# Kernel tuning notes

Hardware: AMD Instinct MI355X
Metric: run time of the kernel (lower is better)

## Reference

```python
import jax, jax.numpy as jnp
import numpy as np

B, IN_DIM, HID, N, ORDER = 128, 2, 64, 1024, 2
NUM_SUPPORTS = 2
IN_TOT = (IN_DIM + HID) * (ORDER * NUM_SUPPORTS + 1)  # 66*5 = 330


def setup_inputs() -> dict:
    key = jax.random.key(0)
    ks = jax.random.split(key, 6)
    inputs = jax.random.normal(ks[0], (B, IN_DIM, N), jnp.float32)
    hx = jax.random.normal(ks[1], (B, HID, N), jnp.float32)
    # row-stochastic-ish diffusion supports, scaled for numerical sanity
    A0 = jax.random.uniform(ks[2], (N, N), jnp.float32) * (2.0 / N)
    A1 = jax.random.uniform(ks[3], (N, N), jnp.float32) * (2.0 / N)
    # 1x1 Conv1d weights (squeezed kernel dim): (out_ch, in_ch)
    W_ru = jax.random.normal(ks[4], (2 * HID, IN_TOT), jnp.float32) * 0.05
    b_ru = jnp.ones((2 * HID,), jnp.float32)  # bias_start=1.0
    W_C = jax.random.normal(ks[5], (HID, IN_TOT), jnp.float32) * 0.05
    b_C = jnp.zeros((HID,), jnp.float32)  # bias_start=0.0
    return {"inputs": inputs, "hx": hx, "A0": A0, "A1": A1,
            "W_ru": W_ru, "b_ru": b_ru, "W_C": W_C, "b_C": b_C}


def _gcn(x, A, order):
    # Chebyshev-like diffusion recursion; x: (B, F, N), A: (N, N)
    x0 = x
    x1 = jnp.einsum('bfn,mn->bfm', x0, A)
    out = [x1]
    for _ in range(2, order + 1):
        x2 = 2.0 * jnp.einsum('bfn,mn->bfm', x1, A) - x0
        out.append(x2)
        x1, x0 = x2, x1
    return jnp.concatenate(out, axis=-2)  # (B, F*order, N)


def _multi_adj_gnn(x, adjs, W, b, order):
    # concat identity + per-support diffusion stacks, then 1x1 conv over channels
    h = jnp.concatenate([x] + [_gcn(x, A, order) for A in adjs], axis=-2)
    return jnp.einsum('bcn,oc->bon', h, W) + b[None, :, None]


def reference(inputs, hx, A0, A1, W_ru, b_ru, W_C, b_C):
    adjs = (A0, A1)
    x = jnp.concatenate([inputs, hx], axis=-2)            # (B, IN+HID, N)
    ru = jax.nn.sigmoid(_multi_adj_gnn(x, adjs, W_ru, b_ru, ORDER))
    r, u = ru[:, :HID, :], ru[:, HID:, :]
    xc = jnp.concatenate([inputs, r * hx], axis=-2)
    Cc = jnp.tanh(_multi_adj_gnn(xc, adjs, W_C, b_C, ORDER))
    return u * hx + (1.0 - u) * Cc                        # (B, HID, N)
```

## Files before the change

kernel.cpp:

```cpp
#include <hip/hip_runtime.h>

using u16 = unsigned short;
using u32 = unsigned int;
typedef __attribute__((ext_vector_type(8))) __bf16 bf16x8;
typedef __attribute__((ext_vector_type(8))) u16 u16x8;
typedef __attribute__((ext_vector_type(4))) float f32x4;

#define DEVI __device__ __forceinline__

constexpr int BN_ = 128;
constexpr int NN  = 1024;
constexpr int CH  = 66;
constexpr int HD  = 64;
constexpr int RR  = BN_ * CH;
constexpr long RN = (long)RR * NN;
constexpr int KTRUE = 330, KPAD = 352;
constexpr long M2 = (long)NN * NN;

DEVI float bf2f(u16 u) { u32 i = ((u32)u) << 16; float f; __builtin_memcpy(&f, &i, 4); return f; }
DEVI u16 f2bf(float f) { u32 i; __builtin_memcpy(&i, &f, 4); i += 0x7fffu + ((i >> 16) & 1u); return (u16)(i >> 16); }

DEVI void gl_lds16(const void* g, void* l) {
  __builtin_amdgcn_global_load_lds((const __attribute__((address_space(1))) u32*)g,
                                   (__attribute__((address_space(3))) u32*)l, 16, 0, 0);
}

template<bool CHEB>
__global__ __launch_bounds__(256, 2)
void gemm_bt(const u16* __restrict__ Xb, long xz,
             const u16* __restrict__ Ab,
             const u16* __restrict__ X0,
             u16* __restrict__ Yb, long yz)
{
  __shared__ u16 Xs[128 * 32];
  __shared__ u16 Bs[128 * 32];
  const int bid = blockIdx.x;
  const int wg  = (bid & 7) * 132 + (bid >> 3);
  const int z   = wg >= 528;
  const int rem = wg - z * 528;
  const int tm  = rem >> 3, tn = rem & 7;

  const u16* X = Xb + (long)z * xz;
  const u16* A = Ab + (long)z * M2;
  u16*       Y = Yb + (long)z * yz;
  const int tid = threadIdx.x, wv = tid >> 6, ln = tid & 63;

  const int r0  = wv * 16 + (ln >> 2);
  const int kch = (((ln & 3) ^ ((r0 >> 1) & 3))) * 8;
  const u16* gX = X + (long)(tm * 128 + r0) * NN + kch;
  const u16* gA = A + (long)(tn * 128 + r0) * NN + kch;
  u16* lX = &Xs[wv * 512];
  u16* lA = &Bs[wv * 512];

  const int frow = ln & 15;
  const int fk   = ((ln >> 4) ^ ((ln >> 1) & 3)) * 8;
  const int wr = wv >> 1, wc = wv & 1;

  f32x4 acc[4][4] = {};

  for (int k0 = 0; k0 < NN; k0 += 32) {
    gl_lds16(gX + k0,            lX);
    gl_lds16(gX + k0 + 64 * NN,  lX + 2048);
    gl_lds16(gA + k0,            lA);
    gl_lds16(gA + k0 + 64 * NN,  lA + 2048);
    __syncthreads();
    bf16x8 af[4], bfv[4];
#pragma unroll
    for (int m = 0; m < 4; m++) af[m]  = *(const bf16x8*)&Xs[(wr * 64 + m * 16 + frow) * 32 + fk];
#pragma unroll
    for (int n = 0; n < 4; n++) bfv[n] = *(const bf16x8*)&Bs[(wc * 64 + n * 16 + frow) * 32 + fk];
#pragma unroll
    for (int m = 0; m < 4; m++)
#pragma unroll
      for (int n = 0; n < 4; n++)
        acc[m][n] = __builtin_amdgcn_mfma_f32_16x16x32_bf16(af[m], bfv[n], acc[m][n], 0, 0, 0);
    __syncthreads();
  }

  const int colb = tn * 128 + wc * 64 + frow;
  const int rowb = tm * 128 + wr * 64 + (ln >> 4) * 4;
#pragma unroll
  for (int m = 0; m < 4; m++)
#pragma unroll
    for (int n = 0; n < 4; n++) {
      const int col = colb + n * 16;
#pragma unroll
      for (int q = 0; q < 4; q++) {
        const long r = rowb + m * 16 + q;
        float v = acc[m][n][q];
        if (CHEB) v = 2.0f * v - bf2f(X0[r * NN + col]);
        Y[r * NN + col] = f2bf(v);
      }
    }
}

template<int O, bool FINAL>
__global__ __launch_bounds__(512)
void proj_f(const u16* __restrict__ part0, const u16* __restrict__ Yb,
            const u16* __restrict__ W, const float* __restrict__ bias,
            const float* __restrict__ hx, const u16* __restrict__ zpad,
            u16* __restrict__ xcrow, float* __restrict__ ubuf,
            float* __restrict__ outp)
{
  __shared__ u16 LB[23040];
  __shared__ u16 LA[5632];
  const int b = blockIdx.y, n0 = blockIdx.x * 64;
  const int tid = threadIdx.x, wv = tid >> 6, ln = tid & 63;

  const int of  = (O == 128) ? wv : (wv >> 1);
  const int nfb = (O == 128) ? 0  : 2 * (wv & 1);
  constexpr int NF = (O == 128) ? 4 : 2;
  const int frow = ln & 15, klane = ln >> 4;

  const u16* wb = W + (long)(of * 16 + frow) * KPAD + klane * 8;
  bf16x8 wf[11];
#pragma unroll
  for (int t = 0; t < 11; ++t) wf[t] = *(const bf16x8*)(wb + t * 32);

  for (int hf = 0; hf < 2; ++hf)
#pragma unroll 1
    for (int ch = 0; ch < 2; ++ch) {
#pragma unroll
      for (int ii = 0; ii < 2; ++ii) {
        const int i = ii * 8 + wv;
        if (i < 11) {
          const int c = ch * 176 + 16 * i + (ln >> 2);
          const u16* src;
          if (c < KTRUE) {
            const int p = c / 66, f = c - 66 * p;
            const u16* base = (p == 0) ? part0 : (Yb + (long)(p - 1) * RN);
            src = base + (long)(b * CH + f) * NN + n0 + hf * 32 + (ln & 3) * 8;
          } else {
            src = zpad;
          }
          gl_lds16(src, (char*)LA + i * 1024);
        }
      }
      __syncthreads();
#pragma unroll
      for (int it = 0; it < 2; ++it) {
        const int q = it * 512 + tid;
        if (q < 704) {
          const int n = q & 31, cch = q >> 5;
          u16x8 v;
#pragma unroll
          for (int j = 0; j < 8; ++j) v[j] = LA[(cch * 8 + j) * 32 + n];
          *(u16x8*)((char*)LB + (hf * 32 + n) * 720 + ch * 352 + cch * 16) = v;
        }
      }
      __syncthreads();
    }

  f32x4 acc[NF] = {};
#pragma unroll
  for (int t = 0; t < 11; ++t) {
#pragma unroll
    for (int j = 0; j < NF; ++j) {
      const int nf = nfb + j;
      const bf16x8 bt = *(const bf16x8*)((char*)LB + (nf * 16 + frow) * 720 + t * 64 + klane * 16);
      acc[j] = __builtin_amdgcn_mfma_f32_16x16x32_bf16(wf[t], bt, acc[j], 0, 0, 0);
    }
  }

  const int orow = klane * 4;
#pragma unroll
  for (int j = 0; j < NF; ++j) {
    const int nf = nfb + j;
    const int ncol = n0 + nf * 16 + frow;
#pragma unroll
    for (int q = 0; q < 4; ++q) {
      const int o = of * 16 + orow + q;
      const float pre = acc[j][q] + bias[o];
      if (!FINAL) {
        const float sg = 1.0f / (1.0f + __expf(-pre));
        if (o < HD) {
          const float hv = hx[(long)(b * HD + o) * NN + ncol];
          xcrow[(long)(b * CH + 2 + o) * NN + ncol] = f2bf(sg * hv);
        } else {
          ubuf[(long)(b * HD + (o - HD)) * NN + ncol] = sg;
        }
      } else {
        const float e  = __expf(2.0f * pre);
        const float cc = 1.0f - 2.0f / (e + 1.0f);
        const long oi = (long)(b * HD + o) * NN + ncol;
        const float u = ubuf[oi];
        outp[oi] = u * hx[oi] + (1.0f - u) * cc;
      }
    }
  }
}

__global__ void build_x(const float* __restrict__ inp, const float* __restrict__ hx,
                        u16* __restrict__ X, u16* __restrict__ XC)
{
  const int row = blockIdx.x;
  const int b = row / 66, f = row - b * 66;
  const int n0 = threadIdx.x * 4;
  const float* s = (f < 2) ? (inp + (long)(b * 2 + f) * NN) : (hx + (long)(b * HD + f - 2) * NN);
  const float4 v = *(const float4*)(s + n0);
  ushort4 o;
  o.x = f2bf(v.x); o.y = f2bf(v.y); o.z = f2bf(v.z); o.w = f2bf(v.w);
  *(ushort4*)&X[(long)row * NN + n0] = o;
  if (f < 2) *(ushort4*)&XC[(long)row * NN + n0] = o;
}

__global__ void prep(const float* __restrict__ A0, const float* __restrict__ A1,
                     const float* __restrict__ Wru, const float* __restrict__ WC,
                     u16* __restrict__ Abf, u16* __restrict__ Wrub, u16* __restrict__ WCb)
{
  const int gid = blockIdx.x * 256 + threadIdx.x;
  if (gid < 524288) {
    const float* s = (gid < 262144) ? (A0 + (long)gid * 4) : (A1 + (long)(gid - 262144) * 4);
    const float4 v = *(const float4*)s;
    ushort4 o; o.x = f2bf(v.x); o.y = f2bf(v.y); o.z = f2bf(v.z); o.w = f2bf(v.w);
    *(ushort4*)&Abf[(long)gid * 4] = o;
  } else if (gid < 524288 + 128 * KPAD) {
    const int g = gid - 524288;
    const int o = g / KPAD, c = g - o * KPAD;
    Wrub[g] = f2bf(c < KTRUE ? Wru[o * KTRUE + c] : 0.0f);
  } else if (gid < 524288 + 128 * KPAD + 64 * KPAD) {
    const int g = gid - 524288 - 128 * KPAD;
    const int o = g / KPAD, c = g - o * KPAD;
    WCb[g] = f2bf(c < KTRUE ? WC[o * KTRUE + c] : 0.0f);
  }
}

extern "C" void kernel_launch(void* const* d_in, const int* in_sizes, int n_in,
                              void* d_out, int out_size, void* d_ws, size_t ws_size,
                              hipStream_t stream)
{
  const float* inp = (const float*)d_in[0];
  const float* hx  = (const float*)d_in[1];
  const float* A0  = (const float*)d_in[2];
  const float* A1  = (const float*)d_in[3];
  const float* Wru = (const float*)d_in[4];
  const float* bru = (const float*)d_in[5];
  const float* WC  = (const float*)d_in[6];
  const float* bC  = (const float*)d_in[7];
  float* out = (float*)d_out;

  char* ws = (char*)d_ws;
  u16* Abf  = (u16*)(ws);
  u16* Wrub = (u16*)(ws + 4194304);
  u16* WCb  = (u16*)(ws + 4284416);
  u16* zpad = (u16*)(ws + 4329472);
  u16* X    = (u16*)(ws + 4329728);
  u16* XC   = (u16*)(ws + 21631232);
  u16* Yb   = (u16*)(ws + 38932736);
  float* ub = out;

  hipMemsetAsync(zpad, 0, 256, stream);
  prep<<<2312, 256, 0, stream>>>(A0, A1, Wru, WC, Abf, Wrub, WCb);
  build_x<<<RR, 256, 0, stream>>>(inp, hx, X, XC);

  const dim3 gx(16, BN_);
  gemm_bt<false><<<1056, 256, 0, stream>>>(X, 0, Abf, nullptr, Yb, 2 * RN);
  gemm_bt<true ><<<1056, 256, 0, stream>>>(Yb, 2 * RN, Abf, X, Yb + RN, 2 * RN);
  proj_f<128, false><<<gx, 512, 0, stream>>>(X, Yb, Wrub, bru, hx, zpad, XC, ub, nullptr);

  gemm_bt<false><<<1056, 256, 0, stream>>>(XC, 0, Abf, nullptr, Yb, 2 * RN);
  gemm_bt<true ><<<1056, 256, 0, stream>>>(Yb, 2 * RN, Abf, XC, Yb + RN, 2 * RN);
  proj_f<64, true><<<gx, 512, 0, stream>>>(XC, Yb, WCb, bC, hx, zpad, nullptr, ub, out);
}
```

Measured before the change: 407.7 us.

## Precompute 2A²−I operators and triple-buffer GEMM loads with one-shot diffusion

```diff
diff --git a/kernel.cpp b/kernel.cpp
--- a/kernel.cpp
+++ b/kernel.cpp
@@ -25,32 +25,29 @@
                                    (__attribute__((address_space(3))) u32*)l, 16, 0, 0);
 }
 
-template<bool CHEB>
+template<int TMZ, bool SQ>
 __global__ __launch_bounds__(256, 2)
-void gemm_bt(const u16* __restrict__ Xb, long xz,
-             const u16* __restrict__ Ab,
-             const u16* __restrict__ X0,
-             u16* __restrict__ Yb, long yz)
-{
-  __shared__ u16 Xs[128 * 32];
-  __shared__ u16 Bs[128 * 32];
+void gemm_db(const u16* __restrict__ Xb, long xzs,
+             const u16* __restrict__ Ab, long azs,
+             u16* __restrict__ Yb, long ozs)
+{
+  __shared__ u16 L[3 * 8192];
   const int bid = blockIdx.x;
-  const int wg  = (bid & 7) * 132 + (bid >> 3);
-  const int z   = wg >= 528;
-  const int rem = wg - z * 528;
+  const int wg  = (bid & 7) * (gridDim.x >> 3) + (bid >> 3);
+  const int z   = wg / TMZ;
+  const int rem = wg - z * TMZ;
   const int tm  = rem >> 3, tn = rem & 7;
 
-  const u16* X = Xb + (long)z * xz;
-  const u16* A = Ab + (long)z * M2;
-  u16*       Y = Yb + (long)z * yz;
+  const u16* X = Xb + (long)z * xzs;
+  const u16* A = Ab + (long)z * azs;
+  u16*       Y = Yb + (long)z * ozs;
   const int tid = threadIdx.x, wv = tid >> 6, ln = tid & 63;
 
   const int r0  = wv * 16 + (ln >> 2);
   const int kch = (((ln & 3) ^ ((r0 >> 1) & 3))) * 8;
   const u16* gX = X + (long)(tm * 128 + r0) * NN + kch;
   const u16* gA = A + (long)(tn * 128 + r0) * NN + kch;
-  u16* lX = &Xs[wv * 512];
-  u16* lA = &Bs[wv * 512];
+  const int lofs = wv * 512;
 
   const int frow = ln & 15;
   const int fk   = ((ln >> 4) ^ ((ln >> 1) & 3)) * 8;
@@ -58,24 +55,47 @@
 
   f32x4 acc[4][4] = {};
 
-  for (int k0 = 0; k0 < NN; k0 += 32) {
-    gl_lds16(gX + k0,            lX);
-    gl_lds16(gX + k0 + 64 * NN,  lX + 2048);
-    gl_lds16(gA + k0,            lA);
-    gl_lds16(gA + k0 + 64 * NN,  lA + 2048);
-    __syncthreads();
+#define STAGE(T, BUF) do {                                  \
+    u16* bx_ = &L[(BUF) * 8192 + lofs];                     \
+    u16* bb_ = &L[(BUF) * 8192 + 4096 + lofs];              \
+    const int k0_ = (T) * 32;                               \
+    gl_lds16(gX + k0_,           bx_);                      \
+    gl_lds16(gX + k0_ + 64 * NN, bx_ + 2048);               \
+    gl_lds16(gA + k0_,           bb_);                      \
+    gl_lds16(gA + k0_ + 64 * NN, bb_ + 2048);               \
+  } while (0)
+
+  STAGE(0, 0);
+  STAGE(1, 1);
+  asm volatile("s_waitcnt vmcnt(4)" ::: "memory");
+  __builtin_amdgcn_s_barrier();
+  __builtin_amdgcn_sched_barrier(0);
+
+  int cur = 0;
+  for (int t = 0; t < 32; ++t) {
+    const int nx = (cur >= 1) ? cur - 1 : cur + 2;
+    if (t + 2 < 32) STAGE(t + 2, nx);
+    const u16* bx = &L[cur * 8192];
+    const u16* bb = bx + 4096;
     bf16x8 af[4], bfv[4];
 #pragma unroll
-    for (int m = 0; m < 4; m++) af[m]  = *(const bf16x8*)&Xs[(wr * 64 + m * 16 + frow) * 32 + fk];
-#pragma unroll
-    for (int n = 0; n < 4; n++) bfv[n] = *(const bf16x8*)&Bs[(wc * 64 + n * 16 + frow) * 32 + fk];
+    for (int m = 0; m < 4; m++) af[m]  = *(const bf16x8*)&bx[(wr * 64 + m * 16 + frow) * 32 + fk];
+#pragma unroll
+    for (int n = 0; n < 4; n++) bfv[n] = *(const bf16x8*)&bb[(wc * 64 + n * 16 + frow) * 32 + fk];
 #pragma unroll
     for (int m = 0; m < 4; m++)
 #pragma unroll
       for (int n = 0; n < 4; n++)
         acc[m][n] = __builtin_amdgcn_mfma_f32_16x16x32_bf16(af[m], bfv[n], acc[m][n], 0, 0, 0);
-    __syncthreads();
+    if (t < 31) {
+      if (t + 2 < 32) asm volatile("s_waitcnt vmcnt(4)" ::: "memory");
+      else            asm volatile("s_waitcnt vmcnt(0)" ::: "memory");
+      __builtin_amdgcn_s_barrier();
+      __builtin_amdgcn_sched_barrier(0);
+    }
+    cur = (cur >= 2) ? 0 : cur + 1;
   }
+#undef STAGE
 
   const int colb = tn * 128 + wc * 64 + frow;
   const int rowb = tm * 128 + wr * 64 + (ln >> 4) * 4;
@@ -88,7 +108,7 @@
       for (int q = 0; q < 4; q++) {
         const long r = rowb + m * 16 + q;
         float v = acc[m][n][q];
-        if (CHEB) v = 2.0f * v - bf2f(X0[r * NN + col]);
+        if (SQ) v = 2.0f * v - (r == col ? 1.0f : 0.0f);
         Y[r * NN + col] = f2bf(v);
       }
     }
@@ -204,16 +224,43 @@
   if (f < 2) *(ushort4*)&XC[(long)row * NN + n0] = o;
 }
 
+__global__ void xposeA(const float* __restrict__ A0, const float* __restrict__ A1,
+                       u16* __restrict__ AT)
+{
+  __shared__ float Ls[64][65];
+  const int z = blockIdx.z;
+  const float* A = z ? A1 : A0;
+  u16* out = AT + (long)z * M2;
+  const int m0 = blockIdx.y * 64, n0 = blockIdx.x * 64;
+  const int t = threadIdx.x;
+  const int rr = t >> 6, cc = t & 63;
+#pragma unroll
+  for (int i = 0; i < 16; i++)
+    Ls[i * 4 + rr][cc] = A[(long)(m0 + i * 4 + rr) * NN + n0 + cc];
+  __syncthreads();
+  const int n = t >> 2, mc = (t & 3) * 16;
+  u16 tmp[16];
+#pragma unroll
+  for (int k = 0; k < 16; k++) tmp[k] = f2bf(Ls[mc + k][n]);
+  u16* dst = &out[(long)(n0 + n) * NN + m0 + mc];
+  *(ushort4*)(dst + 0)  = *(ushort4*)&tmp[0];
+  *(ushort4*)(dst + 4)  = *(ushort4*)&tmp[4];
+  *(ushort4*)(dst + 8)  = *(ushort4*)&tmp[8];
+  *(ushort4*)(dst + 12) = *(ushort4*)&tmp[12];
+}
+
 __global__ void prep(const float* __restrict__ A0, const float* __restrict__ A1,
                      const float* __restrict__ Wru, const float* __restrict__ WC,
-                     u16* __restrict__ Abf, u16* __restrict__ Wrub, u16* __restrict__ WCb)
+                     u16* __restrict__ Abf2, u16* __restrict__ Wrub, u16* __restrict__ WCb)
 {
   const int gid = blockIdx.x * 256 + threadIdx.x;
   if (gid < 524288) {
-    const float* s = (gid < 262144) ? (A0 + (long)gid * 4) : (A1 + (long)(gid - 262144) * 4);
+    const bool sec = gid >= 262144;
+    const float* s = sec ? (A1 + (long)(gid - 262144) * 4) : (A0 + (long)gid * 4);
+    u16* d = sec ? (Abf2 + 2 * M2 + (long)(gid - 262144) * 4) : (Abf2 + (long)gid * 4);
     const float4 v = *(const float4*)s;
     ushort4 o; o.x = f2bf(v.x); o.y = f2bf(v.y); o.z = f2bf(v.z); o.w = f2bf(v.w);
-    *(ushort4*)&Abf[(long)gid * 4] = o;
+    *(ushort4*)d = o;
   } else if (gid < 524288 + 128 * KPAD) {
     const int g = gid - 524288;
     const int o = g / KPAD, c = g - o * KPAD;
@@ -240,25 +287,27 @@
   float* out = (float*)d_out;
 
   char* ws = (char*)d_ws;
-  u16* Abf  = (u16*)(ws);
-  u16* Wrub = (u16*)(ws + 4194304);
-  u16* WCb  = (u16*)(ws + 4284416);
-  u16* zpad = (u16*)(ws + 4329472);
-  u16* X    = (u16*)(ws + 4329728);
-  u16* XC   = (u16*)(ws + 21631232);
-  u16* Yb   = (u16*)(ws + 38932736);
+  u16* Abf2 = (u16*)(ws);
+  u16* ATbf = (u16*)(ws + 8388608);
+  u16* Wrub = (u16*)(ws + 12582912);
+  u16* WCb  = (u16*)(ws + 12673024);
+  u16* zpad = (u16*)(ws + 12718080);
+  u16* X    = (u16*)(ws + 12718336);
+  u16* XC   = (u16*)(ws + 30019840);
+  u16* Yb   = (u16*)(ws + 47321344);
   float* ub = out;
 
   hipMemsetAsync(zpad, 0, 256, stream);
-  prep<<<2312, 256, 0, stream>>>(A0, A1, Wru, WC, Abf, Wrub, WCb);
+  prep<<<2312, 256, 0, stream>>>(A0, A1, Wru, WC, Abf2, Wrub, WCb);
+  xposeA<<<dim3(16, 16, 2), 256, 0, stream>>>(A0, A1, ATbf);
   build_x<<<RR, 256, 0, stream>>>(inp, hx, X, XC);
 
+  gemm_db<64, true><<<128, 256, 0, stream>>>(Abf2, 2 * M2, ATbf, M2, Abf2 + M2, 2 * M2);
+
   const dim3 gx(16, BN_);
-  gemm_bt<false><<<1056, 256, 0, stream>>>(X, 0, Abf, nullptr, Yb, 2 * RN);
-  gemm_bt<true ><<<1056, 256, 0, stream>>>(Yb, 2 * RN, Abf, X, Yb + RN, 2 * RN);
+  gemm_db<528, false><<<2112, 256, 0, stream>>>(X, 0, Abf2, M2, Yb, RN);
   proj_f<128, false><<<gx, 512, 0, stream>>>(X, Yb, Wrub, bru, hx, zpad, XC, ub, nullptr);
 
-  gemm_bt<false><<<1056, 256, 0, stream>>>(XC, 0, Abf, nullptr, Yb, 2 * RN);
-  gemm_bt<true ><<<1056, 256, 0, stream>>>(Yb, 2 * RN, Abf, XC, Yb + RN, 2 * RN);
+  gemm_db<528, false><<<2112, 256, 0, stream>>>(XC, 0, Abf2, M2, Yb, RN);
   proj_f<64, true><<<gx, 512, 0, stream>>>(XC, Yb, WCb, bC, hx, zpad, nullptr, ub, out);
 }
```

After: 373.4 us. 1.09x faster.
